# Performance work log

Measured on AMD Instinct MI355X. Metric: run time of the kernel, lower is better.

## Reference

```python
import jax, jax.numpy as jnp
import numpy as np

SCALING = 32.0 / 16.0  # alpha / rank

def setup_inputs() -> dict:
    key = jax.random.key(0)
    k1, k2, k3, k4 = jax.random.split(key, 4)
    B_, S, D_in, D_out, R = 4, 4096, 2048, 2048, 16
    x = jax.random.normal(k1, (B_, S, D_in), dtype=jnp.float32)
    # dequantized 4-bit base weight, torch Linear layout [out, in]
    W_base = jax.random.normal(k2, (D_out, D_in), dtype=jnp.float32) * 0.02
    A = jax.random.normal(k3, (R, D_in), dtype=jnp.float32) * (1.0 / np.sqrt(D_in))
    # torch code zero-inits lora_B, but use random for nontrivial gradient checking
    B = jax.random.normal(k4, (D_out, R), dtype=jnp.float32) * 0.02
    return {"x": x, "W_base": W_base, "A": A, "B": B}

def reference(x, W_base, A, B):
    # base: Y = x @ W_base^T   [b, s, out]
    base = jnp.einsum('bsd,od->bso', x, W_base)
    # LoRA: (x @ A^T) @ B^T * scaling   (rank is tiny, keep factored)
    lora = jnp.einsum('bsr,or->bso', jnp.einsum('bsd,rd->bsr', x, A), B)
    return base + lora * SCALING
```

## Files before the change

kernel.cpp:

```cpp
#include <hip/hip_runtime.h>


typedef __bf16 bf16x8 __attribute__((ext_vector_type(8)));
typedef float  f32x4  __attribute__((ext_vector_type(4)));
typedef unsigned short u16x8 __attribute__((ext_vector_type(8)));

#define AS1C(p) ((const __attribute__((address_space(1))) void*)(p))
#define AS3(p)  ((__attribute__((address_space(3))) void*)(p))

__device__ __forceinline__ unsigned short f2bf_rne(float f) {
  unsigned int u = __float_as_uint(f);
  u += 0x7FFFu + ((u >> 16) & 1u);
  return (unsigned short)(u >> 16);
}

constexpr int M_ = 16384;
constexpr int N_ = 2048;
constexpr int K_ = 2048;
constexpr int R_ = 16;
constexpr float SCALING = 2.0f;

constexpr int BM = 256, BN = 256, BK = 64;
constexpr int NT = K_ / BK;

__global__ __launch_bounds__(256) void cvt_kernel(const float* __restrict__ in,
                                                  unsigned short* __restrict__ out) {
  size_t i = (size_t)blockIdx.x * blockDim.x + threadIdx.x;
  const float4* p = (const float4*)in;
  float4 a = p[2 * i];
  float4 b = p[2 * i + 1];
  u16x8 o;
  o[0] = f2bf_rne(a.x); o[1] = f2bf_rne(a.y); o[2] = f2bf_rne(a.z); o[3] = f2bf_rne(a.w);
  o[4] = f2bf_rne(b.x); o[5] = f2bf_rne(b.y); o[6] = f2bf_rne(b.z); o[7] = f2bf_rne(b.w);
  ((u16x8*)out)[i] = o;
}

__global__ __launch_bounds__(256) void weff_kernel(const float* __restrict__ W,
                                                   const float* __restrict__ A,
                                                   const float* __restrict__ Bl,
                                                   unsigned short* __restrict__ out) {
  int idx = blockIdx.x * blockDim.x + threadIdx.x;
  int o = idx >> 11;
  int d = idx & 2047;
  float acc = W[idx];
#pragma unroll
  for (int r = 0; r < R_; ++r)
    acc = fmaf(SCALING * Bl[o * R_ + r], A[r * K_ + d], acc);
  out[idx] = f2bf_rne(acc);
}

__global__ __launch_bounds__(512, 2) void gemm_kernel(const unsigned short* __restrict__ X,
                                                      const unsigned short* __restrict__ W,
                                                      float* __restrict__ C) {
  __shared__ __align__(16) unsigned short sA[2][BM * BK];
  __shared__ __align__(16) unsigned short sB[2][BN * BK];

  const int tid  = threadIdx.x;
  const int w    = tid >> 6;
  const int lane = tid & 63;
  const int fm   = lane & 15;
  const int quad = lane >> 4;

  const int id = blockIdx.x;
  const int bm = ((id & 7) * 8 + (id >> 6)) * BM;
  const int bn = ((id >> 3) & 7) * BN;

  const int wrow = (w >> 2) * 128;
  const int wcol = (w & 3) * 64;

  const int strow = tid >> 3;
  const int gseg  = ((tid & 7) - strow) & 7;
  const int brow0 = 64 * (tid >> 8) + (strow & 31);

  const unsigned short* xa = X + (size_t)(bm + strow) * K_ + gseg * 8;
  const unsigned short* xb = W + (size_t)(bn + brow0) * K_ + gseg * 8;

  const int aw = w * 8 * BK;
  const int bw = ((w >> 2) * 64 + (w & 3) * 8) * BK;

  const int sp0 = ((quad + fm) & 7) * 8;
  const int sp1 = ((quad + fm + 4) & 7) * 8;

  f32x4 acc[8][4] = {};
  bf16x8 af[4][2];
  bf16x8 bv0[2][2];
  bf16x8 bv1[2][2];

#define STAGE_A(hm, kt, b) do {                                                   \
    __builtin_amdgcn_global_load_lds(AS1C(xa + (size_t)((hm) * 64) * K_ + (kt) * BK), \
        AS3(&sA[b][((hm) * 64) * BK + aw]), 16, 0, 0);                            \
    __builtin_amdgcn_global_load_lds(AS1C(xa + (size_t)((hm) * 64 + 128) * K_ + (kt) * BK), \
        AS3(&sA[b][((hm) * 64 + 128) * BK + aw]), 16, 0, 0);                      \
  } while (0)

#define STAGE_B(hn, kt, b) do {                                                   \
    __builtin_amdgcn_global_load_lds(AS1C(xb + (size_t)((hn) * 32) * K_ + (kt) * BK), \
        AS3(&sB[b][((hn) * 32) * BK + bw]), 16, 0, 0);                            \
    __builtin_amdgcn_global_load_lds(AS1C(xb + (size_t)((hn) * 32 + 128) * K_ + (kt) * BK), \
        AS3(&sB[b][((hn) * 32 + 128) * BK + bw]), 16, 0, 0);                      \
  } while (0)

#define LOAD_A(hm, tb) do {                                                       \
    _Pragma("unroll")                                                             \
    for (int i2 = 0; i2 < 4; ++i2) {                                              \
      const int ra = (wrow + (hm) * 64 + i2 * 16 + fm) * BK;                      \
      af[i2][0] = *(const bf16x8*)&sA[tb][ra + sp0];                              \
      af[i2][1] = *(const bf16x8*)&sA[tb][ra + sp1];                              \
    }                                                                             \
  } while (0)

#define LOAD_B(bv, hn, tb) do {                                                   \
    _Pragma("unroll")                                                             \
    for (int j2 = 0; j2 < 2; ++j2) {                                              \
      const int rb = (wcol + (hn) * 32 + j2 * 16 + fm) * BK;                      \
      bv[j2][0] = *(const bf16x8*)&sB[tb][rb + sp0];                              \
      bv[j2][1] = *(const bf16x8*)&sB[tb][rb + sp1];                              \
    }                                                                             \
  } while (0)

#define MFMA_Q(hm, hn, bv) do {                                                   \
    __builtin_amdgcn_s_setprio(1);                                                \
    _Pragma("unroll")                                                             \
    for (int ks = 0; ks < 2; ++ks)                                                \
      _Pragma("unroll")                                                           \
      for (int i2 = 0; i2 < 4; ++i2)                                              \
        _Pragma("unroll")                                                         \
        for (int j2 = 0; j2 < 2; ++j2)                                            \
          acc[(hm) * 4 + i2][(hn) * 2 + j2] = __builtin_amdgcn_mfma_f32_16x16x32_bf16( \
              af[i2][ks], (bv)[j2][ks], acc[(hm) * 4 + i2][(hn) * 2 + j2], 0, 0, 0); \
    __builtin_amdgcn_s_setprio(0);                                                \
  } while (0)

#define PH_BAR __builtin_amdgcn_s_barrier()
#define LGKM0  asm volatile("s_waitcnt lgkmcnt(0)" ::: "memory")
#define VMC6   asm volatile("s_waitcnt vmcnt(6)" ::: "memory")

  STAGE_A(0, 0, 0);
  STAGE_B(0, 0, 0);
  STAGE_B(1, 0, 0);
  STAGE_A(1, 0, 0);
  STAGE_A(0, 1, 1);
  STAGE_B(0, 1, 1);
  STAGE_B(1, 1, 1);
  VMC6;
  PH_BAR;

#pragma unroll 1
  for (int it = 0; it < NT / 2; ++it) {
    const int t1 = 2 * it + 1;
    const int t2 = (2 * it + 2 < NT) ? 2 * it + 2 : NT - 1;
    const int t3 = (2 * it + 3 < NT) ? 2 * it + 3 : NT - 1;

    LOAD_A(0, 0); LOAD_B(bv0, 0, 0);
    STAGE_A(1, t1, 1);
    PH_BAR; LGKM0; MFMA_Q(0, 0, bv0); PH_BAR;
    LOAD_B(bv1, 1, 0);
    STAGE_A(0, t2, 0);
    PH_BAR; LGKM0; MFMA_Q(0, 1, bv1); PH_BAR;
    LOAD_A(1, 0);
    STAGE_B(0, t2, 0);
    PH_BAR; LGKM0; MFMA_Q(1, 1, bv1); PH_BAR;
    STAGE_B(1, t2, 0);
    PH_BAR; MFMA_Q(1, 0, bv0); VMC6; PH_BAR;

    LOAD_A(0, 1); LOAD_B(bv0, 0, 1);
    STAGE_A(1, t2, 0);
    PH_BAR; LGKM0; MFMA_Q(0, 0, bv0); PH_BAR;
    LOAD_B(bv1, 1, 1);
    STAGE_A(0, t3, 1);
    PH_BAR; LGKM0; MFMA_Q(0, 1, bv1); PH_BAR;
    LOAD_A(1, 1);
    STAGE_B(0, t3, 1);
    PH_BAR; LGKM0; MFMA_Q(1, 1, bv1); PH_BAR;
    STAGE_B(1, t3, 1);
    PH_BAR; MFMA_Q(1, 0, bv0); VMC6; PH_BAR;
  }

  asm volatile("s_waitcnt vmcnt(0)" ::: "memory");

  const int r0 = quad * 4;
#pragma unroll
  for (int i = 0; i < 8; ++i) {
#pragma unroll
    for (int j = 0; j < 4; ++j) {
      size_t base = (size_t)(bm + wrow + i * 16 + r0) * N_ + (size_t)(bn + wcol + j * 16 + fm);
#pragma unroll
      for (int r = 0; r < 4; ++r)
        __builtin_nontemporal_store(acc[i][j][r], &C[base + (size_t)r * N_]);
    }
  }
#undef PH_BAR
#undef LGKM0
#undef VMC6
#undef MFMA_Q
#undef LOAD_A
#undef LOAD_B
#undef STAGE_A
#undef STAGE_B
}

extern "C" void kernel_launch(void* const* d_in, const int* in_sizes, int n_in,
                              void* d_out, int out_size, void* d_ws, size_t ws_size,
                              hipStream_t stream) {
  const float* x  = (const float*)d_in[0];
  const float* W  = (const float*)d_in[1];
  const float* A  = (const float*)d_in[2];
  const float* Bl = (const float*)d_in[3];
  float* out = (float*)d_out;

  unsigned short* Xb   = (unsigned short*)d_ws;
  unsigned short* Weff = Xb + (size_t)M_ * K_;

  cvt_kernel<<<(int)((size_t)M_ * K_ / 8 / 256), 256, 0, stream>>>(x, Xb);
  weff_kernel<<<(N_ * K_) / 256, 256, 0, stream>>>(W, A, Bl, Weff);

  gemm_kernel<<<(M_ / BM) * (N_ / BN), 512, 0, stream>>>(Xb, Weff, out);
}
```

Measured before the change: 379.9 us.

## Software-pipeline LDS fragment reads ahead of MFMA and halve barriers

```diff
diff --git a/kernel.cpp b/kernel.cpp
--- a/kernel.cpp
+++ b/kernel.cpp
@@ -132,7 +132,7 @@
   } while (0)
 
 #define PH_BAR __builtin_amdgcn_s_barrier()
-#define LGKM0  asm volatile("s_waitcnt lgkmcnt(0)" ::: "memory")
+#define VMC4   asm volatile("s_waitcnt vmcnt(4)" ::: "memory")
 #define VMC6   asm volatile("s_waitcnt vmcnt(6)" ::: "memory")
 
   STAGE_A(0, 0, 0);
@@ -144,6 +144,7 @@
   STAGE_B(1, 1, 1);
   VMC6;
   PH_BAR;
+  LOAD_A(0, 0); LOAD_B(bv0, 0, 0);
 
 #pragma unroll 1
   for (int it = 0; it < NT / 2; ++it) {
@@ -151,29 +152,39 @@
     const int t2 = (2 * it + 2 < NT) ? 2 * it + 2 : NT - 1;
     const int t3 = (2 * it + 3 < NT) ? 2 * it + 3 : NT - 1;
 
+    MFMA_Q(0, 0, bv0);
+    LOAD_B(bv1, 1, 0);
+    STAGE_A(1, t1, 1);
+    PH_BAR;
+    MFMA_Q(0, 1, bv1);
+    LOAD_A(1, 0);
+    STAGE_A(0, t2, 0);
+    PH_BAR;
+    MFMA_Q(1, 1, bv1);
+    STAGE_B(0, t2, 0);
+    VMC4;
+    PH_BAR;
+    MFMA_Q(1, 0, bv0);
+    LOAD_A(0, 1); LOAD_B(bv0, 0, 1);
+    STAGE_B(1, t2, 0);
+    PH_BAR;
+
+    MFMA_Q(0, 0, bv0);
+    LOAD_B(bv1, 1, 1);
+    STAGE_A(1, t2, 0);
+    PH_BAR;
+    MFMA_Q(0, 1, bv1);
+    LOAD_A(1, 1);
+    STAGE_A(0, t3, 1);
+    PH_BAR;
+    MFMA_Q(1, 1, bv1);
+    STAGE_B(0, t3, 1);
+    VMC4;
+    PH_BAR;
+    MFMA_Q(1, 0, bv0);
     LOAD_A(0, 0); LOAD_B(bv0, 0, 0);
-    STAGE_A(1, t1, 1);
-    PH_BAR; LGKM0; MFMA_Q(0, 0, bv0); PH_BAR;
-    LOAD_B(bv1, 1, 0);
-    STAGE_A(0, t2, 0);
-    PH_BAR; LGKM0; MFMA_Q(0, 1, bv1); PH_BAR;
-    LOAD_A(1, 0);
-    STAGE_B(0, t2, 0);
-    PH_BAR; LGKM0; MFMA_Q(1, 1, bv1); PH_BAR;
-    STAGE_B(1, t2, 0);
-    PH_BAR; MFMA_Q(1, 0, bv0); VMC6; PH_BAR;
-
-    LOAD_A(0, 1); LOAD_B(bv0, 0, 1);
-    STAGE_A(1, t2, 0);
-    PH_BAR; LGKM0; MFMA_Q(0, 0, bv0); PH_BAR;
-    LOAD_B(bv1, 1, 1);
-    STAGE_A(0, t3, 1);
-    PH_BAR; LGKM0; MFMA_Q(0, 1, bv1); PH_BAR;
-    LOAD_A(1, 1);
-    STAGE_B(0, t3, 1);
-    PH_BAR; LGKM0; MFMA_Q(1, 1, bv1); PH_BAR;
     STAGE_B(1, t3, 1);
-    PH_BAR; MFMA_Q(1, 0, bv0); VMC6; PH_BAR;
+    PH_BAR;
   }
 
   asm volatile("s_waitcnt vmcnt(0)" ::: "memory");
@@ -190,7 +201,7 @@
     }
   }
 #undef PH_BAR
-#undef LGKM0
+#undef VMC4
 #undef VMC6
 #undef MFMA_Q
 #undef LOAD_A
```

Measured after the change: 376.2 us. About the same (-1.0%).
